# Kernel tuning notes

Hardware: AMD Instinct MI355X
Metric: run time of the kernel (lower is better)

The kernel has to match this reference:

```python
import jax, jax.numpy as jnp
import numpy as np

N, D, P, H = 4096, 128, 128, 256  # n samples, input_dim, pe_dim, hidden_dim


def setup_inputs() -> dict:
    key = jax.random.key(0)
    k0, k1, k2 = jax.random.split(key, 3)
    x = jax.random.normal(k0, (N, D), dtype=jnp.float32)
    # shared_net params: Linear(D+P -> H), Linear(H -> 1)
    W1 = jax.random.normal(k1, (D + P, H), dtype=jnp.float32) / np.sqrt(D + P).astype(np.float32)
    b1 = jnp.zeros((H,), dtype=jnp.float32)
    W2 = jax.random.normal(k2, (H, 1), dtype=jnp.float32) / np.sqrt(H).astype(np.float32)
    b2 = jnp.zeros((1,), dtype=jnp.float32)
    return {"x": x, "W1": W1, "b1": b1, "W2": W2, "b2": b2}


def reference(x, W1, b1, W2, b2):
    """Vectorized NIMO.forward: all d feature-masked MLP evals in one batched GEMM.

    Original python loop: for each j, zero column j of x, append one-hot pe[:, :P],
    run shared MLP -> g_j (n,), column j of B is x[:, j] * (1 + g_j).
    Output B has shape (n, d+1) with a leading ones column.
    Dropout(noise_std=0.0) is identity.
    """
    n, d = x.shape
    p = W1.shape[0] - d
    dt = x.dtype
    # (d, n, d): x replicated d times with column j zeroed in slice j
    mask = (1.0 - jnp.eye(d)).astype(dt)
    x_masked = x[None, :, :] * mask[:, None, :]
    # First linear layer, split into masked-x part and (constant per j) pe part.
    h = jnp.einsum('jni,ih->jnh', x_masked, W1[:d])          # (d, n, h)
    pe_add = jnp.eye(d, dtype=dt)[:, :p] @ W1[d:]            # (d, h): one-hot pe through W1
    h = jax.nn.relu(h + pe_add[:, None, :] + b1)
    g = jnp.einsum('jnh,ho->jno', h, W2)[..., 0] + b2[0]     # (d, n)
    cols = x * (1.0 + g.T)                                   # (n, d)
    return jnp.concatenate([jnp.ones((n, 1), dtype=dt), cols], axis=1)  # (n, d+1)
```

## Files before the change

### kernel.cpp

```cpp
#include <hip/hip_runtime.h>


#define NROWS 4096
#define DIN   128
#define HDIM  256
#define JCH   8

typedef float sfloat16 __attribute__((ext_vector_type(16)));

__global__ __launch_bounds__(256) void nimo_base(
    const float* __restrict__ x, const float* __restrict__ W1,
    const float* __restrict__ b1, float* __restrict__ baseb)
{
    __shared__ float xs[DIN * 36];
    const int tid  = threadIdx.x;
    const int row0 = blockIdx.x * 32;
    const int h0   = blockIdx.y * 64;

    {
        const int bidx = tid * 16;
        const int r = bidx >> 7;
        const int c = bidx & 127;
        #pragma unroll
        for (int u = 0; u < 4; ++u) {
            const float4 v = *(const float4*)(x + (size_t)(row0 + r) * DIN + c + u * 4);
            xs[(c + u * 4 + 0) * 36 + r] = v.x;
            xs[(c + u * 4 + 1) * 36 + r] = v.y;
            xs[(c + u * 4 + 2) * 36 + r] = v.z;
            xs[(c + u * 4 + 3) * 36 + r] = v.w;
        }
    }
    __syncthreads();

    const int tx = tid & 31;
    const int ty = tid >> 5;
    const float* __restrict__ wcol = W1 + h0 + tx * 2;

    float2 acc[4];
    #pragma unroll
    for (int u = 0; u < 4; ++u) { acc[u].x = 0.f; acc[u].y = 0.f; }

    #pragma unroll 8
    for (int k = 0; k < DIN; ++k) {
        const float2 w  = *(const float2*)(wcol + (size_t)k * HDIM);
        const float4 xv = *(const float4*)(&xs[k * 36 + ty * 4]);
        acc[0].x = fmaf(xv.x, w.x, acc[0].x); acc[0].y = fmaf(xv.x, w.y, acc[0].y);
        acc[1].x = fmaf(xv.y, w.x, acc[1].x); acc[1].y = fmaf(xv.y, w.y, acc[1].y);
        acc[2].x = fmaf(xv.z, w.x, acc[2].x); acc[2].y = fmaf(xv.z, w.y, acc[2].y);
        acc[3].x = fmaf(xv.w, w.x, acc[3].x); acc[3].y = fmaf(xv.w, w.y, acc[3].y);
    }

    const float2 bv = *(const float2*)(b1 + h0 + tx * 2);
    #pragma unroll
    for (int u = 0; u < 4; ++u) {
        float2 o; o.x = acc[u].x + bv.x; o.y = acc[u].y + bv.y;
        *(float2*)(baseb + (size_t)(row0 + ty * 4 + u) * HDIM + h0 + tx * 2) = o;
    }
}

__global__ __launch_bounds__(1024, 8) void nimo_main(
    const float* __restrict__ x, const float* __restrict__ W1,
    const float* __restrict__ W2, const float* __restrict__ b2,
    const float* __restrict__ baseb, float* __restrict__ out)
{
    __shared__ float xs[64][JCH + 1];
    __shared__ float part[16][JCH][66];

    const int tid  = threadIdx.x;
    const int r    = tid & 63;
    const int q    = tid >> 6;
    const int row0 = blockIdx.x * 64;
    const int row  = row0 + r;
    const int j0   = blockIdx.y * JCH;
    const int h0   = q * 16;

    if (tid < 512) {
        const int xr = tid >> 3;
        const int xc = tid & 7;
        xs[xr][xc] = x[(size_t)(row0 + xr) * DIN + j0 + xc];
    }

    float bb[16], w2r[16];
    {
        const float4* bp  = (const float4*)(baseb + (size_t)row * HDIM + h0);
        const float4* wp2 = (const float4*)(W2 + h0);
        #pragma unroll
        for (int u = 0; u < 4; ++u) {
            const float4 v = bp[u];
            bb[u * 4 + 0] = v.x; bb[u * 4 + 1] = v.y;
            bb[u * 4 + 2] = v.z; bb[u * 4 + 3] = v.w;
            const float4 w = wp2[u];
            w2r[u * 4 + 0] = w.x; w2r[u * 4 + 1] = w.y;
            w2r[u * 4 + 2] = w.z; w2r[u * 4 + 3] = w.w;
        }
    }
    __syncthreads();

    for (int jj = 0; jj < JCH; ++jj) {
        const float xj = xs[r][jj];
        unsigned off = (unsigned)(((j0 + jj) * HDIM + h0) * 4);
        off = __builtin_amdgcn_readfirstlane(off);
        sfloat16 wa, wp;
        asm volatile(
            "s_load_dwordx16 %0, %2, 0x0\n\t"
            "s_load_dwordx16 %1, %2, 0x20000\n\t"
            "s_waitcnt lgkmcnt(0)"
            : "=s"(wa), "=s"(wp)
            : "s"((unsigned long long)(uintptr_t)W1 + off));

        float acc = 0.f;
        #pragma unroll
        for (int h = 0; h < 16; ++h) {
            float t = bb[h] + wp[h];
            t = fmaf(-xj, wa[h], t);
            t = fmaxf(t, 0.f);
            acc = fmaf(t, w2r[h], acc);
        }
        part[q][jj][r] = acc;
    }
    __syncthreads();

    const float b2s = b2[0];
    if (blockIdx.y == 0 && tid < 64) out[(size_t)(row0 + tid) * 129] = 1.0f;

    if (tid < 512) {
        const int rr = tid >> 3;
        const int jj = tid & 7;
        float g = 0.f;
        #pragma unroll
        for (int qq = 0; qq < 16; ++qq) g += part[qq][jj][rr];
        const float xv = xs[rr][jj];
        out[(size_t)(row0 + rr) * 129 + 1 + j0 + jj] = xv * (1.0f + g + b2s);
    }
}

extern "C" void kernel_launch(void* const* d_in, const int* in_sizes, int n_in,
                              void* d_out, int out_size, void* d_ws, size_t ws_size,
                              hipStream_t stream) {
    const float* x  = (const float*)d_in[0];
    const float* W1 = (const float*)d_in[1];
    const float* b1 = (const float*)d_in[2];
    const float* W2 = (const float*)d_in[3];
    const float* b2 = (const float*)d_in[4];
    float* out = (float*)d_out;
    float* baseb = (float*)d_ws;

    nimo_base<<<dim3(NROWS / 32, HDIM / 64), 256, 0, stream>>>(x, W1, b1, baseb);
    nimo_main<<<dim3(NROWS / 64, DIN / JCH), 1024, 0, stream>>>(x, W1, W2, b2, baseb, out);
}
```

Measured before the change: 87.87 us.

## Split base GEMM over K into two partials and pair j-iterations in main kernel

```diff
diff --git a/kernel.cpp b/kernel.cpp
--- a/kernel.cpp
+++ b/kernel.cpp
@@ -12,18 +12,20 @@
     const float* __restrict__ x, const float* __restrict__ W1,
     const float* __restrict__ b1, float* __restrict__ baseb)
 {
-    __shared__ float xs[DIN * 36];
+    __shared__ float xs[64 * 36];
     const int tid  = threadIdx.x;
     const int row0 = blockIdx.x * 32;
     const int h0   = blockIdx.y * 64;
+    const int k0   = blockIdx.z * 64;
+    float* __restrict__ pbuf = baseb + (size_t)blockIdx.z * (NROWS * HDIM);
 
     {
-        const int bidx = tid * 16;
-        const int r = bidx >> 7;
-        const int c = bidx & 127;
+        const int bidx = tid * 8;
+        const int r = bidx >> 6;
+        const int c = bidx & 63;
         #pragma unroll
-        for (int u = 0; u < 4; ++u) {
-            const float4 v = *(const float4*)(x + (size_t)(row0 + r) * DIN + c + u * 4);
+        for (int u = 0; u < 2; ++u) {
+            const float4 v = *(const float4*)(x + (size_t)(row0 + r) * DIN + k0 + c + u * 4);
             xs[(c + u * 4 + 0) * 36 + r] = v.x;
             xs[(c + u * 4 + 1) * 36 + r] = v.y;
             xs[(c + u * 4 + 2) * 36 + r] = v.z;
@@ -34,14 +36,14 @@
 
     const int tx = tid & 31;
     const int ty = tid >> 5;
-    const float* __restrict__ wcol = W1 + h0 + tx * 2;
+    const float* __restrict__ wcol = W1 + (size_t)k0 * HDIM + h0 + tx * 2;
 
     float2 acc[4];
     #pragma unroll
     for (int u = 0; u < 4; ++u) { acc[u].x = 0.f; acc[u].y = 0.f; }
 
     #pragma unroll 8
-    for (int k = 0; k < DIN; ++k) {
+    for (int k = 0; k < 64; ++k) {
         const float2 w  = *(const float2*)(wcol + (size_t)k * HDIM);
         const float4 xv = *(const float4*)(&xs[k * 36 + ty * 4]);
         acc[0].x = fmaf(xv.x, w.x, acc[0].x); acc[0].y = fmaf(xv.x, w.y, acc[0].y);
@@ -50,11 +52,12 @@
         acc[3].x = fmaf(xv.w, w.x, acc[3].x); acc[3].y = fmaf(xv.w, w.y, acc[3].y);
     }
 
-    const float2 bv = *(const float2*)(b1 + h0 + tx * 2);
+    float2 bv = make_float2(0.f, 0.f);
+    if (blockIdx.z == 0) bv = *(const float2*)(b1 + h0 + tx * 2);
     #pragma unroll
     for (int u = 0; u < 4; ++u) {
         float2 o; o.x = acc[u].x + bv.x; o.y = acc[u].y + bv.y;
-        *(float2*)(baseb + (size_t)(row0 + ty * 4 + u) * HDIM + h0 + tx * 2) = o;
+        *(float2*)(pbuf + (size_t)(row0 + ty * 4 + u) * HDIM + h0 + tx * 2) = o;
     }
 }
 
@@ -82,13 +85,15 @@
 
     float bb[16], w2r[16];
     {
-        const float4* bp  = (const float4*)(baseb + (size_t)row * HDIM + h0);
+        const float4* a0  = (const float4*)(baseb + (size_t)row * HDIM + h0);
+        const float4* a1  = (const float4*)(baseb + (size_t)NROWS * HDIM + (size_t)row * HDIM + h0);
         const float4* wp2 = (const float4*)(W2 + h0);
         #pragma unroll
         for (int u = 0; u < 4; ++u) {
-            const float4 v = bp[u];
-            bb[u * 4 + 0] = v.x; bb[u * 4 + 1] = v.y;
-            bb[u * 4 + 2] = v.z; bb[u * 4 + 3] = v.w;
+            const float4 v0 = a0[u];
+            const float4 v1 = a1[u];
+            bb[u * 4 + 0] = v0.x + v1.x; bb[u * 4 + 1] = v0.y + v1.y;
+            bb[u * 4 + 2] = v0.z + v1.z; bb[u * 4 + 3] = v0.w + v1.w;
             const float4 w = wp2[u];
             w2r[u * 4 + 0] = w.x; w2r[u * 4 + 1] = w.y;
             w2r[u * 4 + 2] = w.z; w2r[u * 4 + 3] = w.w;
@@ -96,27 +101,36 @@
     }
     __syncthreads();
 
-    for (int jj = 0; jj < JCH; ++jj) {
-        const float xj = xs[r][jj];
-        unsigned off = (unsigned)(((j0 + jj) * HDIM + h0) * 4);
+    #pragma unroll
+    for (int jp = 0; jp < JCH; jp += 2) {
+        unsigned off = (unsigned)(((j0 + jp) * HDIM + h0) * 4);
         off = __builtin_amdgcn_readfirstlane(off);
-        sfloat16 wa, wp;
+        sfloat16 wa0, wp0, wa1, wp1;
         asm volatile(
-            "s_load_dwordx16 %0, %2, 0x0\n\t"
-            "s_load_dwordx16 %1, %2, 0x20000\n\t"
+            "s_load_dwordx16 %0, %4, 0x0\n\t"
+            "s_load_dwordx16 %1, %4, 0x20000\n\t"
+            "s_load_dwordx16 %2, %4, 0x400\n\t"
+            "s_load_dwordx16 %3, %4, 0x20400\n\t"
             "s_waitcnt lgkmcnt(0)"
-            : "=s"(wa), "=s"(wp)
+            : "=s"(wa0), "=s"(wp0), "=s"(wa1), "=s"(wp1)
             : "s"((unsigned long long)(uintptr_t)W1 + off));
 
-        float acc = 0.f;
+        const float xj0 = xs[r][jp];
+        const float xj1 = xs[r][jp + 1];
+        float acc0 = 0.f, acc1 = 0.f;
         #pragma unroll
         for (int h = 0; h < 16; ++h) {
-            float t = bb[h] + wp[h];
-            t = fmaf(-xj, wa[h], t);
-            t = fmaxf(t, 0.f);
-            acc = fmaf(t, w2r[h], acc);
+            float t0 = bb[h] + wp0[h];
+            t0 = fmaf(-xj0, wa0[h], t0);
+            t0 = fmaxf(t0, 0.f);
+            acc0 = fmaf(t0, w2r[h], acc0);
+            float t1 = bb[h] + wp1[h];
+            t1 = fmaf(-xj1, wa1[h], t1);
+            t1 = fmaxf(t1, 0.f);
+            acc1 = fmaf(t1, w2r[h], acc1);
         }
-        part[q][jj][r] = acc;
+        part[q][jp][r]     = acc0;
+        part[q][jp + 1][r] = acc1;
     }
     __syncthreads();
 
@@ -145,6 +159,6 @@
     float* out = (float*)d_out;
     float* baseb = (float*)d_ws;
 
-    nimo_base<<<dim3(NROWS / 32, HDIM / 64), 256, 0, stream>>>(x, W1, b1, baseb);
+    nimo_base<<<dim3(NROWS / 32, HDIM / 64, 2), 256, 0, stream>>>(x, W1, b1, baseb);
     nimo_main<<<dim3(NROWS / 64, DIN / JCH), 1024, 0, stream>>>(x, W1, W2, b2, baseb, out);
 }
```

Result: slower. 95.52 us (+8.7%).

## Process 256 rows per block in nimo_main to amortize scalar weight loads

Applied to the files above, without the earlier changes.

```diff
diff --git a/kernel.cpp b/kernel.cpp
--- a/kernel.cpp
+++ b/kernel.cpp
@@ -5,6 +5,7 @@
 #define DIN   128
 #define HDIM  256
 #define JCH   8
+#define RPB   256
 
 typedef float sfloat16 __attribute__((ext_vector_type(16)));
 
@@ -58,79 +59,100 @@
     }
 }
 
-__global__ __launch_bounds__(1024, 8) void nimo_main(
+__global__ __launch_bounds__(1024, 4) void nimo_main(
     const float* __restrict__ x, const float* __restrict__ W1,
     const float* __restrict__ W2, const float* __restrict__ b2,
     const float* __restrict__ baseb, float* __restrict__ out)
 {
-    __shared__ float xs[64][JCH + 1];
-    __shared__ float part[16][JCH][66];
+    __shared__ float xs[RPB][JCH + 1];
+    __shared__ float part[16][2][RPB + 2];
 
     const int tid  = threadIdx.x;
-    const int r    = tid & 63;
+    const int lane = tid & 63;
     const int q    = tid >> 6;
-    const int row0 = blockIdx.x * 64;
-    const int row  = row0 + r;
+    const int row0 = blockIdx.x * RPB;
     const int j0   = blockIdx.y * JCH;
     const int h0   = q * 16;
 
-    if (tid < 512) {
-        const int xr = tid >> 3;
-        const int xc = tid & 7;
-        xs[xr][xc] = x[(size_t)(row0 + xr) * DIN + j0 + xc];
+    {
+        const int rr = tid >> 2;
+        const int jc = (tid & 3) * 2;
+        const float2 v = *(const float2*)(x + (size_t)(row0 + rr) * DIN + j0 + jc);
+        xs[rr][jc] = v.x; xs[rr][jc + 1] = v.y;
     }
 
-    float bb[16], w2r[16];
-    {
-        const float4* bp  = (const float4*)(baseb + (size_t)row * HDIM + h0);
-        const float4* wp2 = (const float4*)(W2 + h0);
+    unsigned w2off = __builtin_amdgcn_readfirstlane((unsigned)(h0 * 4));
+    sfloat16 w2s;
+    asm volatile(
+        "s_load_dwordx16 %0, %1, 0x0\n\t"
+        "s_waitcnt lgkmcnt(0)"
+        : "=s"(w2s) : "s"((unsigned long long)(uintptr_t)W2 + w2off));
+
+    float bb[64];
+    #pragma unroll
+    for (int g = 0; g < 4; ++g) {
+        const float* bp = baseb + (size_t)(row0 + g * 64 + lane) * HDIM + h0;
         #pragma unroll
         for (int u = 0; u < 4; ++u) {
-            const float4 v = bp[u];
-            bb[u * 4 + 0] = v.x; bb[u * 4 + 1] = v.y;
-            bb[u * 4 + 2] = v.z; bb[u * 4 + 3] = v.w;
-            const float4 w = wp2[u];
-            w2r[u * 4 + 0] = w.x; w2r[u * 4 + 1] = w.y;
-            w2r[u * 4 + 2] = w.z; w2r[u * 4 + 3] = w.w;
+            const float4 v = *(const float4*)(bp + u * 4);
+            bb[g * 16 + u * 4 + 0] = v.x; bb[g * 16 + u * 4 + 1] = v.y;
+            bb[g * 16 + u * 4 + 2] = v.z; bb[g * 16 + u * 4 + 3] = v.w;
         }
     }
+
+    const float b2s = b2[0];
+    if (blockIdx.y == 0 && tid < RPB) out[(size_t)(row0 + tid) * 129] = 1.0f;
+
+    unsigned off0 = __builtin_amdgcn_readfirstlane((unsigned)((j0 * HDIM + h0) * 4));
+    const unsigned long long wbase = (unsigned long long)(uintptr_t)W1 + off0;
     __syncthreads();
 
-    for (int jj = 0; jj < JCH; ++jj) {
-        const float xj = xs[r][jj];
-        unsigned off = (unsigned)(((j0 + jj) * HDIM + h0) * 4);
-        off = __builtin_amdgcn_readfirstlane(off);
-        sfloat16 wa, wp;
+    #pragma unroll
+    for (int jb = 0; jb < JCH; jb += 2) {
+        sfloat16 wa0, wp0, wa1, wp1;
         asm volatile(
-            "s_load_dwordx16 %0, %2, 0x0\n\t"
-            "s_load_dwordx16 %1, %2, 0x20000\n\t"
+            "s_load_dwordx16 %0, %4, %5\n\t"
+            "s_load_dwordx16 %1, %4, %6\n\t"
+            "s_load_dwordx16 %2, %4, %7\n\t"
+            "s_load_dwordx16 %3, %4, %8\n\t"
             "s_waitcnt lgkmcnt(0)"
-            : "=s"(wa), "=s"(wp)
-            : "s"((unsigned long long)(uintptr_t)W1 + off));
+            : "=s"(wa0), "=s"(wp0), "=s"(wa1), "=s"(wp1)
+            : "s"(wbase),
+              "i"(jb * 0x400),           "i"(0x20000 + jb * 0x400),
+              "i"((jb + 1) * 0x400),     "i"(0x20000 + (jb + 1) * 0x400));
 
-        float acc = 0.f;
         #pragma unroll
-        for (int h = 0; h < 16; ++h) {
-            float t = bb[h] + wp[h];
-            t = fmaf(-xj, wa[h], t);
-            t = fmaxf(t, 0.f);
-            acc = fmaf(t, w2r[h], acc);
+        for (int s = 0; s < 2; ++s) {
+            const int jj = jb + s;
+            #pragma unroll
+            for (int g = 0; g < 4; ++g) {
+                const float xj = xs[g * 64 + lane][jj];
+                float acc = 0.f;
+                #pragma unroll
+                for (int h = 0; h < 16; ++h) {
+                    const float wph = s ? wp1[h] : wp0[h];
+                    const float wah = s ? wa1[h] : wa0[h];
+                    float t = bb[g * 16 + h] + wph;
+                    t = fmaf(-xj, wah, t);
+                    t = fmaxf(t, 0.f);
+                    acc = fmaf(t, w2s[h], acc);
+                }
+                part[q][s][g * 64 + lane] = acc;
+            }
         }
-        part[q][jj][r] = acc;
-    }
-    __syncthreads();
+        __syncthreads();
 
-    const float b2s = b2[0];
-    if (blockIdx.y == 0 && tid < 64) out[(size_t)(row0 + tid) * 129] = 1.0f;
-
-    if (tid < 512) {
-        const int rr = tid >> 3;
-        const int jj = tid & 7;
-        float g = 0.f;
-        #pragma unroll
-        for (int qq = 0; qq < 16; ++qq) g += part[qq][jj][rr];
-        const float xv = xs[rr][jj];
-        out[(size_t)(row0 + rr) * 129 + 1 + j0 + jj] = xv * (1.0f + g + b2s);
+        if (tid < 512) {
+            const int rr = tid & 255;
+            const int ss = tid >> 8;
+            float gsum = 0.f;
+            #pragma unroll
+            for (int qq = 0; qq < 16; ++qq) gsum += part[qq][ss][rr];
+            const float xvv = xs[rr][jb + ss];
+            out[(size_t)(row0 + rr) * 129 + 1 + j0 + jb + ss] =
+                xvv * (1.0f + gsum + b2s);
+        }
+        __syncthreads();
     }
 }
 
@@ -146,5 +168,5 @@
     float* baseb = (float*)d_ws;
 
     nimo_base<<<dim3(NROWS / 32, HDIM / 64), 256, 0, stream>>>(x, W1, b1, baseb);
-    nimo_main<<<dim3(NROWS / 64, DIN / JCH), 1024, 0, stream>>>(x, W1, W2, b2, baseb, out);
+    nimo_main<<<dim3(NROWS / RPB, DIN / JCH), 1024, 0, stream>>>(x, W1, W2, b2, baseb, out);
 }
```

New measurement: 95.65 us. 8.9% more time.
